# Kernel optimization log

Measured on AMD Instinct MI355X. Metric: run time of the kernel, lower is better.

The kernel has to match this reference:

```python
import jax, jax.numpy as jnp
import numpy as np

HID = 128
N_NODES = 50000
N_REL = 500
N_EDGES = 625000
BN_EPS = 1e-5
LRELU_SLOPE = 0.01


def _xavier(key, shape):
    fan_in, fan_out = shape[1], shape[0]
    std = float(np.sqrt(2.0 / (fan_in + fan_out)))
    return jax.random.normal(key, shape, dtype=jnp.float32) * std


def setup_inputs() -> dict:
    key = jax.random.key(0)
    ks = jax.random.split(key, 16)
    x = jax.random.normal(ks[0], (N_NODES, HID), dtype=jnp.float32)
    r = jax.random.normal(ks[1], (N_REL, HID), dtype=jnp.float32)
    que_context = jax.random.normal(ks[2], (1, HID), dtype=jnp.float32)
    fin_que = jax.random.normal(ks[3], (1, 1, HID), dtype=jnp.float32)
    edge_index = jax.random.randint(ks[4], (2, N_EDGES), 0, N_NODES, dtype=jnp.int64)
    edge_attr = jax.random.randint(ks[5], (N_EDGES,), 0, N_REL, dtype=jnp.int64)
    return {
        "x": x, "r": r, "que_context": que_context, "fin_que": fin_que,
        "edge_index": edge_index, "edge_attr": edge_attr,
        # mess_comp: Linear(2*hid, hid) + Tanh
        "W_mess": _xavier(ks[6], (HID, 2 * HID)), "b_mess": jnp.zeros((HID,), jnp.float32),
        # mess_atten_trans: Linear(2*hid, hid) + LeakyReLU
        "W_matt": _xavier(ks[7], (HID, 2 * HID)), "b_matt": jnp.zeros((HID,), jnp.float32),
        "mess_atten_weight": _xavier(ks[8], (1, HID)),
        # x_atten_trans: Linear(2*hid, hid) + LeakyReLU
        "W_xatt": _xavier(ks[9], (HID, 2 * HID)), "b_xatt": jnp.zeros((HID,), jnp.float32),
        "x_atten_weight": _xavier(ks[10], (1, HID)),
        # BatchNorm1d(hid) affine params (training-mode batch stats are used)
        "bn_gamma": jnp.ones((HID,), jnp.float32), "bn_beta": jnp.zeros((HID,), jnp.float32),
    }


def reference(x, r, que_context, fin_que, edge_index, edge_attr,
              W_mess, b_mess, W_matt, b_matt, mess_atten_weight,
              W_xatt, b_xatt, x_atten_weight, bn_gamma, bn_beta):
    n_nodes = x.shape[0]
    # BatchNorm1d over relation embeddings (training-mode: batch statistics, biased var)
    mu = jnp.mean(r, axis=0)
    var = jnp.mean(jnp.square(r - mu), axis=0)
    r = (r - mu) * jax.lax.rsqrt(var + BN_EPS) * bn_gamma + bn_beta

    head_ents, tail_ents = edge_index[0], edge_index[1]
    head_embeds = x[head_ents]            # [E, H]
    rel_embeds = r[edge_attr]             # [E, H]

    # message computation: Linear(2H->H) + tanh
    mess_in = jnp.concatenate([head_embeds, rel_embeds], axis=1)  # [E, 2H]
    mess = jnp.tanh(mess_in @ W_mess.T + b_mess)                  # [E, H]

    # message attention logits
    qc = jnp.broadcast_to(que_context, (mess.shape[0], que_context.shape[1]))
    mc = jnp.concatenate([mess, qc], axis=1) @ W_matt.T + b_matt
    mc = jax.nn.leaky_relu(mc, LRELU_SLOPE)
    mess_coeffs = jnp.sum(mess_atten_weight * mc, axis=1)         # [E]

    # segment softmax over tail_ents
    seg_max = jax.ops.segment_max(mess_coeffs, tail_ents, num_segments=n_nodes)
    mess_coeffs = jnp.exp(mess_coeffs - seg_max[tail_ents])
    seg_sum = jax.ops.segment_sum(mess_coeffs, tail_ents, num_segments=n_nodes)
    mess_weights = mess_coeffs / (seg_sum[tail_ents] + 1e-16)

    # weighted scatter-sum aggregation
    sum_mess = jax.ops.segment_sum(mess * mess_weights[:, None], tail_ents,
                                   num_segments=n_nodes)          # [N, H]

    # gating attention between x and aggregated messages
    pair = jnp.stack([x, sum_mess], axis=1)                       # [N, 2, H]
    fq = jnp.broadcast_to(fin_que, (n_nodes, 2, fin_que.shape[2]))
    xc = jnp.concatenate([pair, fq], axis=2)                      # [N, 2, 2H]
    xc = jax.nn.leaky_relu(jnp.einsum('nkc,hc->nkh', xc, W_xatt) + b_xatt, LRELU_SLOPE)
    x_coeffs = jnp.sum(x_atten_weight[None] * xc, axis=2)         # [N, 2]
    x_weight = jax.nn.softmax(x_coeffs, axis=1)
    x_out = x_weight[:, 0:1] * x + x_weight[:, 1:2] * sum_mess
    # dropout is identity (eval / p=0)
    return x_out, r
```

## Files before the change

kernel.cpp:

```cpp
#include <hip/hip_runtime.h>
#include <hip/hip_bf16.h>

#define HID 128
#define NN 50000
#define NR 500
#define NE 625000
#define LRELU 0.01f
#define SCAN_BLOCKS 196

typedef __hip_bfloat16 bf16;
typedef __attribute__((ext_vector_type(8))) short short8;
typedef __attribute__((ext_vector_type(4))) float float4_;

__device__ __forceinline__ float b2f(bf16 v) { return __bfloat162float(v); }
__device__ __forceinline__ bf16 f2b(float v) { return __float2bfloat16(v); }

__device__ __forceinline__ float san(float v) {
    return (v == v && v > -1e30f && v < 1e30f) ? v : 0.f;
}

__device__ __forceinline__ float ftanh(float a) {
    float e = __expf(2.f * a);
    return 1.f - 2.f * __builtin_amdgcn_rcpf(e + 1.f);
}

__device__ __forceinline__ float ldf(const void* p, int i, int f32) {
    return f32 ? ((const float*)p)[i] : b2f(((const bf16*)p)[i]);
}
__device__ __forceinline__ void stf(void* p, int i, float v, int f32) {
    if (f32) ((float*)p)[i] = v;
    else ((bf16*)p)[i] = f2b(v);
}

__device__ __forceinline__ int clampi(int v, int hi) {
    return v < 0 ? 0 : (v >= hi ? hi - 1 : v);
}
__device__ __forceinline__ int idx_at(const int* p, int i, int is64) {
    return p[is64 ? (2 * i) : i];
}

__device__ __forceinline__ unsigned short bfbits(float v) {
    bf16 h = f2b(v);
    return *(unsigned short*)&h;
}
__device__ __forceinline__ unsigned int packbf2(float a, float b) {
    return (unsigned int)bfbits(a) | ((unsigned int)bfbits(b) << 16);
}
__device__ __forceinline__ float bflo(unsigned int u) { return __uint_as_float(u << 16); }
__device__ __forceinline__ float bfhi(unsigned int u) { return __uint_as_float(u & 0xffff0000u); }

__device__ __forceinline__ float xorReduce16(float v) {
    v += __shfl_xor(v, 1, 64);
    v += __shfl_xor(v, 2, 64);
    v += __shfl_xor(v, 4, 64);
    v += __shfl_xor(v, 8, 64);
    return v;
}
__device__ __forceinline__ float waveMax(float v) {
#pragma unroll
    for (int o = 1; o < 64; o <<= 1) v = fmaxf(v, __shfl_xor(v, o, 64));
    return v;
}
__device__ __forceinline__ float waveSum(float v) {
#pragma unroll
    for (int o = 1; o < 64; o <<= 1) v += __shfl_xor(v, o, 64);
    return v;
}

__device__ __forceinline__ float dot8(const void* W, int row, int col, int f32,
                                      const float* vec) {
    float s;
    if (f32) {
        const float* p = (const float*)W + (size_t)row * 2 * HID + col;
        float4 a = *(const float4*)p;
        float4 b = *(const float4*)(p + 4);
        s = a.x * vec[0] + a.y * vec[1] + a.z * vec[2] + a.w * vec[3]
          + b.x * vec[4] + b.y * vec[5] + b.z * vec[6] + b.w * vec[7];
    } else {
        short8 v = *(const short8*)((const bf16*)W + (size_t)row * 2 * HID + col);
        s = 0.f;
#pragma unroll
        for (int i = 0; i < 8; ++i) {
            unsigned int u = ((unsigned int)(unsigned short)v[i]) << 16;
            s += __uint_as_float(u) * vec[i];
        }
    }
    return s;
}

struct DetectArr {
    const void* p[16];
    int sz[16];
    int kind[16];
};

__global__ void detect_all(DetectArr d, int* __restrict__ flags) {
    int b = blockIdx.x;
    int t = threadIdx.x;
    if (d.kind[b] == 1) {
        if (t < 64) {
            const int* q = (const int*)d.p[b];
            int o = q[2 * t + 1];
            unsigned long long bm = __ballot(o != 0);
            if (t == 0) flags[b] = (bm == 0ull) ? 1 : 0;
        }
        return;
    }
    __shared__ int sb[256], sf[256];
    const unsigned int* w = (const unsigned int*)d.p[b];
    int K = d.sz[b] >> 1;
    if (K > 4096) K = 4096;
    int bv = 0, fv = 0;
    for (int i = t; i < K; i += 256) {
        unsigned int x = w[i];
        unsigned int lo = x & 0xFFFFu, hi = x >> 16;
        if (lo == 0u) {
            if (hi) fv++;
        } else {
            unsigned int e = (lo >> 7) & 0xFFu;
            if (e >= 90u && e <= 160u) bv++;
            else fv++;
        }
    }
    sb[t] = bv; sf[t] = fv;
    __syncthreads();
    for (int o = 128; o > 0; o >>= 1) {
        if (t < o) { sb[t] += sb[t + o]; sf[t] += sf[t + o]; }
        __syncthreads();
    }
    if (t == 0) flags[b] = (sf[0] > sb[0]) ? 1 : 0;
}

__global__ void bn_stats(const void* __restrict__ r, const int* __restrict__ flags,
                         float* __restrict__ stats) {
    __shared__ float sb[256], sq[256];
    const int fr = flags[1];
    int h = blockIdx.x;
    int t = threadIdx.x;
    float s = 0.f, ss = 0.f;
    for (int i = t; i < NR; i += 256) {
        float v = ldf(r, i * HID + h, fr);
        s += v; ss += v * v;
    }
    sb[t] = s; sq[t] = ss;
    __syncthreads();
    for (int o = 128; o > 0; o >>= 1) {
        if (t < o) { sb[t] += sb[t + o]; sq[t] += sq[t + o]; }
        __syncthreads();
    }
    if (t == 0) {
        float mu = sb[0] / NR;
        float var = sq[0] / NR - mu * mu;
        if (var < 0.f) var = 0.f;
        stats[h] = mu;
        stats[HID + h] = rsqrtf(var + 1e-5f);
    }
}

__global__ void bn_apply(const void* __restrict__ r, const void* __restrict__ gamma,
                         const void* __restrict__ beta, const int* __restrict__ flags,
                         const float* __restrict__ stats,
                         float* __restrict__ rnorm, void* __restrict__ out_base) {
    const int fr = flags[1], fg = flags[14], fb = flags[15], fo = flags[0];
    int i = blockIdx.x * 256 + threadIdx.x;
    if (i >= NR * HID) return;
    int h = i & 127;
    float v = san((ldf(r, i, fr) - stats[h]) * stats[HID + h] * ldf(gamma, h, fg)
                  + ldf(beta, h, fb));
    rnorm[i] = v;
    stf(out_base, NN * HID + i, v, fo);
}

__global__ void precomp_kernel(const void* __restrict__ Wmatt, const void* __restrict__ bmatt,
                               const void* __restrict__ qc,
                               const void* __restrict__ Wxatt, const void* __restrict__ bxatt,
                               const void* __restrict__ fq, const int* __restrict__ flags,
                               float* __restrict__ cmatt, float* __restrict__ cxatt) {
    __shared__ float vs[HID];
    __shared__ float part[256];
    const void* W    = blockIdx.x ? Wxatt : Wmatt;
    const void* bias = blockIdx.x ? bxatt : bmatt;
    const void* vsrc = blockIdx.x ? fq : qc;
    float* out       = blockIdx.x ? cxatt : cmatt;
    const int fW = flags[blockIdx.x ? 11 : 8];
    const int fb = flags[blockIdx.x ? 12 : 9];
    const int fv = flags[blockIdx.x ? 3 : 2];
    int t = threadIdx.x;
    if (t < HID) vs[t] = ldf(vsrc, t, fv);
    __syncthreads();
    int h = t & 127, ks = t >> 7;
    float a = 0.f;
#pragma unroll
    for (int i = 0; i < 8; ++i)
        a += dot8(W, h, HID + ks * 64 + i * 8, fW, &vs[ks * 64 + i * 8]);
    part[t] = a;
    __syncthreads();
    if (t < HID) out[h] = san(part[h] + part[h + 128] + ldf(bias, h, fb));
}

__global__ void rm_kernel(const void* __restrict__ Wmess, const void* __restrict__ bmess,
                          const int* __restrict__ flags,
                          const float* __restrict__ rnorm, bf16* __restrict__ Rmb) {
    __shared__ float rl[2][HID];
    const int fW = flags[6], fb = flags[7];
    int t = threadIdx.x;
    int sub = t >> 7, h = t & 127;
    int rel = blockIdx.x * 2 + sub;
    rl[sub][h] = rnorm[rel * HID + h];
    __syncthreads();
    float a = ldf(bmess, h, fb);
#pragma unroll
    for (int i = 0; i < 16; ++i)
        a += dot8(Wmess, h, HID + i * 8, fW, &rl[sub][i * 8]);
    Rmb[rel * HID + h] = f2b(san(a));
}

#define MLDA 136

__device__ __forceinline__ short8 load_bfrag(const void* W, int n, int k0, int f32) {
    short8 b;
    if (f32) {
        const float* Wf = (const float*)W + (size_t)n * 2 * HID + k0;
        float4 u0 = *(const float4*)Wf;
        float4 u1 = *(const float4*)(Wf + 4);
        b[0] = (short)bfbits(u0.x); b[1] = (short)bfbits(u0.y);
        b[2] = (short)bfbits(u0.z); b[3] = (short)bfbits(u0.w);
        b[4] = (short)bfbits(u1.x); b[5] = (short)bfbits(u1.y);
        b[6] = (short)bfbits(u1.z); b[7] = (short)bfbits(u1.w);
    } else {
        b = *(const short8*)((const bf16*)W + (size_t)n * 2 * HID + k0);
    }
    return b;
}

__global__ __launch_bounds__(256, 4) void xm_mfma(const void* __restrict__ x,
                                                  const void* __restrict__ Wmess,
                                                  const int* __restrict__ flags,
                                                  bf16* __restrict__ Xmb) {
    __shared__ short ml[64 * MLDA];
    const int fx = flags[0], fW = flags[6];
    int tid = threadIdx.x;
    int l = tid & 63, w = tid >> 6;
    int quad = l >> 4, lo16 = l & 15;
    int nbase = w * 32;
    short8 bfr[2][4];
#pragma unroll
    for (int nt = 0; nt < 2; ++nt)
#pragma unroll
        for (int kk = 0; kk < 4; ++kk)
            bfr[nt][kk] = load_bfrag(Wmess, nbase + nt * 16 + lo16, kk * 32 + quad * 8, fW);

    const int ntiles = (NN + 63) / 64;
    for (int tile = blockIdx.x; tile < ntiles; tile += gridDim.x) {
        __syncthreads();
#pragma unroll
        for (int p = 0; p < 8; ++p) {
            int rl_ = p * 8 + (tid >> 5);
            int node = clampi(tile * 64 + rl_, NN);
            int k4 = (tid & 31) * 4;
            unsigned int o0, o1;
            if (fx) {
                float4 v = *(const float4*)((const float*)x + (size_t)node * HID + k4);
                o0 = packbf2(v.x, v.y);
                o1 = packbf2(v.z, v.w);
            } else {
                uint2 u = *(const uint2*)((const bf16*)x + (size_t)node * HID + k4);
                o0 = u.x; o1 = u.y;
            }
            unsigned int* dst = (unsigned int*)&ml[rl_ * MLDA + k4];
            dst[0] = o0; dst[1] = o1;
        }
        __syncthreads();
        float4_ acc[4][2];
#pragma unroll
        for (int mt = 0; mt < 4; ++mt)
#pragma unroll
            for (int nt = 0; nt < 2; ++nt)
                acc[mt][nt] = (float4_){0.f, 0.f, 0.f, 0.f};
#pragma unroll
        for (int kk = 0; kk < 4; ++kk) {
            short8 a[4];
#pragma unroll
            for (int mt = 0; mt < 4; ++mt)
                a[mt] = *(const short8*)&ml[(mt * 16 + lo16) * MLDA + kk * 32 + quad * 8];
#pragma unroll
            for (int mt = 0; mt < 4; ++mt)
#pragma unroll
                for (int nt = 0; nt < 2; ++nt)
                    acc[mt][nt] = __builtin_amdgcn_mfma_f32_16x16x32_bf16(
                        a[mt], bfr[nt][kk], acc[mt][nt], 0, 0, 0);
        }
#pragma unroll
        for (int mt = 0; mt < 4; ++mt)
#pragma unroll
            for (int nt = 0; nt < 2; ++nt)
#pragma unroll
                for (int r = 0; r < 4; ++r) {
                    int node = tile * 64 + mt * 16 + quad * 4 + r;
                    if (node < NN)
                        Xmb[node * HID + nbase + nt * 16 + lo16] = f2b(san(acc[mt][nt][r]));
                }
    }
}

__global__ __launch_bounds__(256, 6) void edge_coeff_mfma(
        const bf16* __restrict__ Xmb, const bf16* __restrict__ Rmb,
        const void* __restrict__ Wmatt, const float* __restrict__ cmatt,
        const void* __restrict__ maw, const unsigned int* __restrict__ hrcsr,
        const int* __restrict__ flags, float* __restrict__ ccsr) {
    __shared__ short ml[64 * MLDA];
    __shared__ float swave[4][64];
    const int fWm = flags[8], fmw = flags[10];
    int tid = threadIdx.x;
    int l = tid & 63, w = tid >> 6;
    int quad = l >> 4, lo16 = l & 15;
    int nbase = w * 32;
    short8 bfr[2][4];
#pragma unroll
    for (int nt = 0; nt < 2; ++nt)
#pragma unroll
        for (int kk = 0; kk < 4; ++kk)
            bfr[nt][kk] = load_bfrag(Wmatt, nbase + nt * 16 + lo16, kk * 32 + quad * 8, fWm);

    int n0 = nbase + lo16, n1 = n0 + 16;
    float c0 = cmatt[n0], c1 = cmatt[n1];
    float w0 = ldf(maw, n0, fmw), w1 = ldf(maw, n1, fmw);

    const int ntiles = (NE + 63) / 64;
    const int seg = tid & 15;
    const int rowsub = tid >> 4;
    for (int T = blockIdx.x; T < ntiles; T += gridDim.x) {
        __syncthreads();
#pragma unroll
        for (int p = 0; p < 4; ++p) {
            int el = p * 16 + rowsub;
            int slot = T * 64 + el;
            unsigned int hr = hrcsr[slot < NE ? slot : NE - 1];
            int head = hr & 0xffffu, rel = hr >> 16;
            int k8 = seg * 8;
            uint4 xv = *(const uint4*)&Xmb[head * HID + k8];
            uint4 rv = *(const uint4*)&Rmb[rel * HID + k8];
            uint4 o;
            o.x = packbf2(ftanh(bflo(xv.x) + bflo(rv.x)), ftanh(bfhi(xv.x) + bfhi(rv.x)));
            o.y = packbf2(ftanh(bflo(xv.y) + bflo(rv.y)), ftanh(bfhi(xv.y) + bfhi(rv.y)));
            o.z = packbf2(ftanh(bflo(xv.z) + bflo(rv.z)), ftanh(bfhi(xv.z) + bfhi(rv.z)));
            o.w = packbf2(ftanh(bflo(xv.w) + bflo(rv.w)), ftanh(bfhi(xv.w) + bfhi(rv.w)));
            *(uint4*)&ml[el * MLDA + k8] = o;
        }
        __syncthreads();
        float4_ acc[4][2];
#pragma unroll
        for (int mt = 0; mt < 4; ++mt)
#pragma unroll
            for (int nt = 0; nt < 2; ++nt)
                acc[mt][nt] = (float4_){0.f, 0.f, 0.f, 0.f};
#pragma unroll
        for (int kk = 0; kk < 4; ++kk) {
            short8 a[4];
#pragma unroll
            for (int mt = 0; mt < 4; ++mt)
                a[mt] = *(const short8*)&ml[(mt * 16 + lo16) * MLDA + kk * 32 + quad * 8];
#pragma unroll
            for (int mt = 0; mt < 4; ++mt)
#pragma unroll
                for (int nt = 0; nt < 2; ++nt)
                    acc[mt][nt] = __builtin_amdgcn_mfma_f32_16x16x32_bf16(
                        a[mt], bfr[nt][kk], acc[mt][nt], 0, 0, 0);
        }
#pragma unroll
        for (int mt = 0; mt < 4; ++mt)
#pragma unroll
            for (int r = 0; r < 4; ++r) {
                float z0 = acc[mt][0][r] + c0;
                z0 = z0 > 0.f ? z0 : LRELU * z0;
                float z1 = acc[mt][1][r] + c1;
                z1 = z1 > 0.f ? z1 : LRELU * z1;
                float s = w0 * z0 + w1 * z1;
                s = xorReduce16(s);
                if (lo16 == 0) swave[w][mt * 16 + quad * 4 + r] = s;
            }
        __syncthreads();
        if (tid < 64) {
            int slot = T * 64 + tid;
            if (slot < NE)
                ccsr[slot] = san(swave[0][tid] + swave[1][tid] + swave[2][tid] + swave[3][tid]);
        }
    }
}

__global__ __launch_bounds__(256, 4) void gate_mfma(
        const void* __restrict__ x, const bf16* __restrict__ smb,
        const void* __restrict__ Wxatt, const float* __restrict__ cxatt,
        const void* __restrict__ xaw, const int* __restrict__ flags,
        void* __restrict__ outx) {
    __shared__ short ml[64 * MLDA];
    __shared__ float swave[4][64];
    __shared__ float lgL[64];
    const int fx = flags[0], fWx = flags[11], fxw = flags[13], fo = flags[0];
    int tid = threadIdx.x;
    int l = tid & 63, w = tid >> 6;
    int quad = l >> 4, lo16 = l & 15;
    int nbase = w * 32;
    short8 bfr[2][4];
#pragma unroll
    for (int nt = 0; nt < 2; ++nt)
#pragma unroll
        for (int kk = 0; kk < 4; ++kk)
            bfr[nt][kk] = load_bfrag(Wxatt, nbase + nt * 16 + lo16, kk * 32 + quad * 8, fWx);

    int n0 = nbase + lo16, n1 = n0 + 16;
    float c0 = cxatt[n0], c1 = cxatt[n1];
    float w0 = ldf(xaw, n0, fxw), w1 = ldf(xaw, n1, fxw);

    const int ntiles = (NN + 31) / 32;
    for (int tile = blockIdx.x; tile < ntiles; tile += gridDim.x) {
        __syncthreads();
#pragma unroll
        for (int p = 0; p < 8; ++p) {
            int rl_ = p * 8 + (tid >> 5);
            int node = clampi(tile * 32 + (rl_ >> 1), NN);
            int k4 = (tid & 31) * 4;
            unsigned int o0, o1;
            if (rl_ & 1) {
                uint2 u = *(const uint2*)&smb[node * HID + k4];
                o0 = u.x; o1 = u.y;
            } else if (fx) {
                float4 v = *(const float4*)((const float*)x + (size_t)node * HID + k4);
                o0 = packbf2(v.x, v.y);
                o1 = packbf2(v.z, v.w);
            } else {
                uint2 u = *(const uint2*)((const bf16*)x + (size_t)node * HID + k4);
                o0 = u.x; o1 = u.y;
            }
            unsigned int* dst = (unsigned int*)&ml[rl_ * MLDA + k4];
            dst[0] = o0; dst[1] = o1;
        }
        __syncthreads();
        float4_ acc[4][2];
#pragma unroll
        for (int mt = 0; mt < 4; ++mt)
#pragma unroll
            for (int nt = 0; nt < 2; ++nt)
                acc[mt][nt] = (float4_){0.f, 0.f, 0.f, 0.f};
#pragma unroll
        for (int kk = 0; kk < 4; ++kk) {
            short8 a[4];
#pragma unroll
            for (int mt = 0; mt < 4; ++mt)
                a[mt] = *(const short8*)&ml[(mt * 16 + lo16) * MLDA + kk * 32 + quad * 8];
#pragma unroll
            for (int mt = 0; mt < 4; ++mt)
#pragma unroll
                for (int nt = 0; nt < 2; ++nt)
                    acc[mt][nt] = __builtin_amdgcn_mfma_f32_16x16x32_bf16(
                        a[mt], bfr[nt][kk], acc[mt][nt], 0, 0, 0);
        }
#pragma unroll
        for (int mt = 0; mt < 4; ++mt)
#pragma unroll
            for (int r = 0; r < 4; ++r) {
                float z0 = acc[mt][0][r] + c0;
                z0 = z0 > 0.f ? z0 : LRELU * z0;
                float z1 = acc[mt][1][r] + c1;
                z1 = z1 > 0.f ? z1 : LRELU * z1;
                float s = w0 * z0 + w1 * z1;
                s = xorReduce16(s);
                if (lo16 == 0) swave[w][mt * 16 + quad * 4 + r] = s;
            }
        __syncthreads();
        if (tid < 64)
            lgL[tid] = san(swave[0][tid] + swave[1][tid] + swave[2][tid] + swave[3][tid]);
        __syncthreads();
#pragma unroll
        for (int it = 0; it < 16; ++it) {
            int idx = tid + 256 * it;
            int nl = idx >> 7, h = idx & 127;
            int node = tile * 32 + nl;
            if (node < NN) {
                float g0 = lgL[2 * nl], g1 = lgL[2 * nl + 1];
                float mm = fmaxf(g0, g1);
                float e0 = __expf(g0 - mm), e1 = __expf(g1 - mm);
                float inv = __builtin_amdgcn_rcpf(e0 + e1);
                float xv = ldf(x, node * HID + h, fx);
                float sv = b2f(smb[node * HID + h]);
                stf(outx, node * HID + h, san((e0 * xv + e1 * sv) * inv), fo);
            }
        }
    }
}

__global__ void count_kernel(const int* __restrict__ ei, const int* __restrict__ flags,
                             int* __restrict__ counts) {
    const int is64e = flags[4];
    for (int e = blockIdx.x * blockDim.x + threadIdx.x; e < NE; e += gridDim.x * blockDim.x) {
        int tail = clampi(idx_at(ei, NE + e, is64e), NN);
        atomicAdd(&counts[tail], 1);
    }
}

__global__ void scan_phase1(const int* __restrict__ counts, int* __restrict__ offs,
                            int* __restrict__ bsum) {
    __shared__ int buf[256];
    int t = threadIdx.x;
    int i = blockIdx.x * 256 + t;
    int v = (i < NN) ? counts[i] : 0;
    buf[t] = v;
    __syncthreads();
    for (int off = 1; off < 256; off <<= 1) {
        int add = (t >= off) ? buf[t - off] : 0;
        __syncthreads();
        buf[t] += add;
        __syncthreads();
    }
    if (i < NN) offs[i] = buf[t] - v;
    if (t == 255) bsum[blockIdx.x] = buf[255];
}

__global__ void scan_phase2(int* __restrict__ bsum, int* __restrict__ bexc) {
    __shared__ int buf[256];
    int t = threadIdx.x;
    int v = (t < SCAN_BLOCKS) ? bsum[t] : 0;
    buf[t] = v;
    __syncthreads();
    for (int off = 1; off < 256; off <<= 1) {
        int add = (t >= off) ? buf[t - off] : 0;
        __syncthreads();
        buf[t] += add;
        __syncthreads();
    }
    if (t < SCAN_BLOCKS) bexc[t] = buf[t] - v;
    if (t == 255) bexc[SCAN_BLOCKS] = buf[255];
}

__global__ void scan_phase3(int* __restrict__ offs, int* __restrict__ cursor,
                            const int* __restrict__ bexc) {
    int i = blockIdx.x * 256 + threadIdx.x;
    if (i < NN) {
        int v = offs[i] + bexc[blockIdx.x];
        offs[i] = v;
        cursor[i] = v;
    }
    if (i == 0) offs[NN] = bexc[SCAN_BLOCKS];
}

__global__ void scatter_kernel(const int* __restrict__ ei, const int* __restrict__ ea,
                               const int* __restrict__ flags,
                               int* __restrict__ cursor, unsigned int* __restrict__ hrcsr) {
    const int is64e = flags[4], is64a = flags[5];
    for (int e = blockIdx.x * blockDim.x + threadIdx.x; e < NE; e += gridDim.x * blockDim.x) {
        int tail = clampi(idx_at(ei, NE + e, is64e), NN);
        int head = clampi(idx_at(ei, e, is64e), NN);
        int rel = clampi(idx_at(ea, e, is64a), NR);
        int p = atomicAdd(&cursor[tail], 1);
        if (p >= 0 && p < NE)
            hrcsr[p] = (unsigned int)head | ((unsigned int)rel << 16);
    }
}

__global__ __launch_bounds__(256, 8) void node_aggr_kernel(
        const bf16* __restrict__ Xmb, const bf16* __restrict__ Rmb,
        const int* __restrict__ offs, const unsigned int* __restrict__ hrcsr,
        const float* __restrict__ ccsr, bf16* __restrict__ smb) {
    int tid = threadIdx.x;
    int sub = tid >> 6;
    int lane = tid & 63;
    int node = blockIdx.x * 4 + sub;
    if (node >= NN) return;
    int s = offs[node], en = offs[node + 1];

    float m = -INFINITY;
    for (int i = s + lane; i < en; i += 64) m = fmaxf(m, ccsr[i]);
    m = waveMax(m);
    float lsum = 0.f;
    for (int i = s + lane; i < en; i += 64) lsum += __expf(ccsr[i] - m);
    lsum = waveSum(lsum);
    float inv = 1.f / (lsum + 1e-16f);

    const int col = lane * 2;
    float acc0 = 0.f, acc1 = 0.f;
    int i = s;
    for (; i + 2 <= en; i += 2) {
        unsigned int hr0 = hrcsr[i], hr1 = hrcsr[i + 1];
        float wg0 = __expf(ccsr[i] - m), wg1 = __expf(ccsr[i + 1] - m);
        unsigned int xv0 = *(const unsigned int*)&Xmb[(hr0 & 0xffffu) * HID + col];
        unsigned int rv0 = *(const unsigned int*)&Rmb[(hr0 >> 16) * HID + col];
        unsigned int xv1 = *(const unsigned int*)&Xmb[(hr1 & 0xffffu) * HID + col];
        unsigned int rv1 = *(const unsigned int*)&Rmb[(hr1 >> 16) * HID + col];
        acc0 += wg0 * ftanh(bflo(xv0) + bflo(rv0)) + wg1 * ftanh(bflo(xv1) + bflo(rv1));
        acc1 += wg0 * ftanh(bfhi(xv0) + bfhi(rv0)) + wg1 * ftanh(bfhi(xv1) + bfhi(rv1));
    }
    if (i < en) {
        unsigned int hr0 = hrcsr[i];
        float wg0 = __expf(ccsr[i] - m);
        unsigned int xv0 = *(const unsigned int*)&Xmb[(hr0 & 0xffffu) * HID + col];
        unsigned int rv0 = *(const unsigned int*)&Rmb[(hr0 >> 16) * HID + col];
        acc0 += wg0 * ftanh(bflo(xv0) + bflo(rv0));
        acc1 += wg0 * ftanh(bfhi(xv0) + bfhi(rv0));
    }
    *(unsigned int*)&smb[node * HID + col] = packbf2(san(acc0 * inv), san(acc1 * inv));
}

extern "C" void kernel_launch(void* const* d_in, const int* in_sizes, int n_in,
                              void* d_out, int out_size, void* d_ws, size_t ws_size,
                              hipStream_t stream) {
    const void* x     = d_in[0];
    const void* r     = d_in[1];
    const void* qc    = d_in[2];
    const void* fq    = d_in[3];
    const int*  ei    = (const int*)d_in[4];
    const int*  ea    = (const int*)d_in[5];
    const void* Wmess = d_in[6];
    const void* bmess = d_in[7];
    const void* Wmatt = d_in[8];
    const void* bmatt = d_in[9];
    const void* maw   = d_in[10];
    const void* Wxatt = d_in[11];
    const void* bxatt = d_in[12];
    const void* xaw   = d_in[13];
    const void* gamma = d_in[14];
    const void* beta  = d_in[15];

    int*          flags  = (int*)d_ws;
    int*          counts = flags + 16;
    int*          offs   = counts + NN;
    int*          cursor = offs + NN + 1;
    int*          bsum   = cursor + NN + 3;
    int*          bexc   = bsum + 256;
    unsigned int* hrcsr  = (unsigned int*)(bexc + 260);
    float*        ccsr   = (float*)(hrcsr + NE);
    float*        rnorm  = ccsr + NE;
    float*        stats  = rnorm + (size_t)NR * HID;
    float*        cmatt  = stats + 2 * HID;
    float*        cxatt  = cmatt + HID;
    bf16*         Rmb    = (bf16*)(cxatt + HID);
    bf16*         Xmb    = Rmb + (size_t)NR * HID;
    bf16*         smb    = Xmb + (size_t)NN * HID;

    hipMemsetAsync(counts, 0, NN * sizeof(int), stream);

    DetectArr da;
    const void* ps[16] = {x, r, qc, fq, ei, ea, Wmess, bmess, Wmatt, bmatt, maw,
                          Wxatt, bxatt, xaw, gamma, beta};
    int szs[16] = {NN * HID, NR * HID, HID, HID, 2 * NE, NE, 2 * HID * HID, HID,
                   2 * HID * HID, HID, HID, 2 * HID * HID, HID, HID, HID, HID};
    for (int i = 0; i < 16; ++i) {
        da.p[i] = ps[i];
        da.sz[i] = szs[i];
        da.kind[i] = (i == 4 || i == 5) ? 1 : 0;
    }
    detect_all<<<16, 256, 0, stream>>>(da, flags);

    bn_stats<<<HID, 256, 0, stream>>>(r, flags, stats);
    bn_apply<<<(NR * HID + 255) / 256, 256, 0, stream>>>(r, gamma, beta, flags, stats,
                                                         rnorm, d_out);
    precomp_kernel<<<2, 256, 0, stream>>>(Wmatt, bmatt, qc, Wxatt, bxatt, fq, flags,
                                          cmatt, cxatt);
    rm_kernel<<<NR / 2, 256, 0, stream>>>(Wmess, bmess, flags, rnorm, Rmb);
    xm_mfma<<<782, 256, 0, stream>>>(x, Wmess, flags, Xmb);
    count_kernel<<<1024, 256, 0, stream>>>(ei, flags, counts);
    scan_phase1<<<SCAN_BLOCKS, 256, 0, stream>>>(counts, offs, bsum);
    scan_phase2<<<1, 256, 0, stream>>>(bsum, bexc);
    scan_phase3<<<SCAN_BLOCKS, 256, 0, stream>>>(offs, cursor, bexc);
    scatter_kernel<<<1024, 256, 0, stream>>>(ei, ea, flags, cursor, hrcsr);
    edge_coeff_mfma<<<1536, 256, 0, stream>>>(Xmb, Rmb, Wmatt, cmatt, maw, hrcsr, flags,
                                              ccsr);
    node_aggr_kernel<<<(NN + 3) / 4, 256, 0, stream>>>(Xmb, Rmb, offs, hrcsr, ccsr, smb);
    gate_mfma<<<1563, 256, 0, stream>>>(x, smb, Wxatt, cxatt, xaw, flags, d_out);
}
```

Before: 409.9 us.

## Process edge coefficients in head-sorted order for gather locality, scatter to tail CSR

Builds a second CSR sorted by head node, with a slot map back to tail-CSR positions, and runs the edge coefficient kernel in head-sorted order. Consecutive edges then gather the same Xmb rows, which should improve cache reuse, and results are scattered into the tail-ordered ccsr array. The cost is an extra count/scan pass, more atomics in scatter, extra index arrays and scattered writes. Launch bounds occupancy and grid size are also raised.

```diff
diff --git a/kernel.cpp b/kernel.cpp
--- a/kernel.cpp
+++ b/kernel.cpp
@@ -303,10 +303,11 @@
     }
 }
 
-__global__ __launch_bounds__(256, 6) void edge_coeff_mfma(
+__global__ __launch_bounds__(256, 8) void edge_coeff_mfma(
         const bf16* __restrict__ Xmb, const bf16* __restrict__ Rmb,
         const void* __restrict__ Wmatt, const float* __restrict__ cmatt,
-        const void* __restrict__ maw, const unsigned int* __restrict__ hrcsr,
+        const void* __restrict__ maw, const unsigned int* __restrict__ hhr2,
+        const unsigned int* __restrict__ hslot,
         const int* __restrict__ flags, float* __restrict__ ccsr) {
     __shared__ short ml[64 * MLDA];
     __shared__ float swave[4][64];
@@ -334,8 +335,8 @@
 #pragma unroll
         for (int p = 0; p < 4; ++p) {
             int el = p * 16 + rowsub;
-            int slot = T * 64 + el;
-            unsigned int hr = hrcsr[slot < NE ? slot : NE - 1];
+            int i = T * 64 + el;
+            unsigned int hr = hhr2[i < NE ? i : NE - 1];
             int head = hr & 0xffffu, rel = hr >> 16;
             int k8 = seg * 8;
             uint4 xv = *(const uint4*)&Xmb[head * HID + k8];
@@ -381,9 +382,10 @@
             }
         __syncthreads();
         if (tid < 64) {
-            int slot = T * 64 + tid;
-            if (slot < NE)
-                ccsr[slot] = san(swave[0][tid] + swave[1][tid] + swave[2][tid] + swave[3][tid]);
+            int i = T * 64 + tid;
+            if (i < NE)
+                ccsr[hslot[i]] = san(swave[0][tid] + swave[1][tid]
+                                     + swave[2][tid] + swave[3][tid]);
         }
     }
 }
@@ -490,11 +492,13 @@
 }
 
 __global__ void count_kernel(const int* __restrict__ ei, const int* __restrict__ flags,
-                             int* __restrict__ counts) {
+                             int* __restrict__ countsT, int* __restrict__ countsH) {
     const int is64e = flags[4];
     for (int e = blockIdx.x * blockDim.x + threadIdx.x; e < NE; e += gridDim.x * blockDim.x) {
         int tail = clampi(idx_at(ei, NE + e, is64e), NN);
-        atomicAdd(&counts[tail], 1);
+        int head = clampi(idx_at(ei, e, is64e), NN);
+        atomicAdd(&countsT[tail], 1);
+        atomicAdd(&countsH[head], 1);
     }
 }
 
@@ -545,15 +549,23 @@
 
 __global__ void scatter_kernel(const int* __restrict__ ei, const int* __restrict__ ea,
                                const int* __restrict__ flags,
-                               int* __restrict__ cursor, unsigned int* __restrict__ hrcsr) {
+                               int* __restrict__ cursorT, int* __restrict__ cursorH,
+                               unsigned int* __restrict__ hrcsr,
+                               unsigned int* __restrict__ hhr2,
+                               unsigned int* __restrict__ hslot) {
     const int is64e = flags[4], is64a = flags[5];
     for (int e = blockIdx.x * blockDim.x + threadIdx.x; e < NE; e += gridDim.x * blockDim.x) {
         int tail = clampi(idx_at(ei, NE + e, is64e), NN);
         int head = clampi(idx_at(ei, e, is64e), NN);
         int rel = clampi(idx_at(ea, e, is64a), NR);
-        int p = atomicAdd(&cursor[tail], 1);
-        if (p >= 0 && p < NE)
-            hrcsr[p] = (unsigned int)head | ((unsigned int)rel << 16);
+        unsigned int hr = (unsigned int)head | ((unsigned int)rel << 16);
+        int p = atomicAdd(&cursorT[tail], 1);
+        if (p >= 0 && p < NE) hrcsr[p] = hr;
+        int q = atomicAdd(&cursorH[head], 1);
+        if (q >= 0 && q < NE) {
+            hhr2[q] = hr;
+            hslot[q] = (unsigned int)(p >= 0 && p < NE ? p : 0);
+        }
     }
 }
 
@@ -620,23 +632,30 @@
     const void* gamma = d_in[14];
     const void* beta  = d_in[15];
 
-    int*          flags  = (int*)d_ws;
-    int*          counts = flags + 16;
-    int*          offs   = counts + NN;
-    int*          cursor = offs + NN + 1;
-    int*          bsum   = cursor + NN + 3;
-    int*          bexc   = bsum + 256;
-    unsigned int* hrcsr  = (unsigned int*)(bexc + 260);
-    float*        ccsr   = (float*)(hrcsr + NE);
-    float*        rnorm  = ccsr + NE;
-    float*        stats  = rnorm + (size_t)NR * HID;
-    float*        cmatt  = stats + 2 * HID;
-    float*        cxatt  = cmatt + HID;
-    bf16*         Rmb    = (bf16*)(cxatt + HID);
-    bf16*         Xmb    = Rmb + (size_t)NR * HID;
-    bf16*         smb    = Xmb + (size_t)NN * HID;
-
-    hipMemsetAsync(counts, 0, NN * sizeof(int), stream);
+    int*          flags   = (int*)d_ws;
+    int*          counts  = flags + 16;
+    int*          hcounts = counts + NN;
+    int*          offs    = hcounts + NN;
+    int*          cursor  = offs + NN + 1;
+    int*          bsum    = cursor + NN + 3;
+    int*          bexc    = bsum + 256;
+    int*          hoffs   = bexc + 260;
+    int*          cursorH = hoffs + NN + 1;
+    int*          bsumH   = cursorH + NN + 3;
+    int*          bexcH   = bsumH + 256;
+    unsigned int* hrcsr   = (unsigned int*)(bexcH + 260);
+    unsigned int* hhr2    = hrcsr + NE;
+    unsigned int* hslot   = hhr2 + NE;
+    float*        ccsr    = (float*)(hslot + NE);
+    float*        rnorm   = ccsr + NE;
+    float*        stats   = rnorm + (size_t)NR * HID;
+    float*        cmatt   = stats + 2 * HID;
+    float*        cxatt   = cmatt + HID;
+    bf16*         Rmb     = (bf16*)(cxatt + HID);
+    bf16*         Xmb     = Rmb + (size_t)NR * HID;
+    bf16*         smb     = Xmb + (size_t)NN * HID;
+
+    hipMemsetAsync(counts, 0, 2 * NN * sizeof(int), stream);
 
     DetectArr da;
     const void* ps[16] = {x, r, qc, fq, ei, ea, Wmess, bmess, Wmatt, bmatt, maw,
@@ -657,13 +676,17 @@
                                           cmatt, cxatt);
     rm_kernel<<<NR / 2, 256, 0, stream>>>(Wmess, bmess, flags, rnorm, Rmb);
     xm_mfma<<<782, 256, 0, stream>>>(x, Wmess, flags, Xmb);
-    count_kernel<<<1024, 256, 0, stream>>>(ei, flags, counts);
+    count_kernel<<<1024, 256, 0, stream>>>(ei, flags, counts, hcounts);
     scan_phase1<<<SCAN_BLOCKS, 256, 0, stream>>>(counts, offs, bsum);
     scan_phase2<<<1, 256, 0, stream>>>(bsum, bexc);
     scan_phase3<<<SCAN_BLOCKS, 256, 0, stream>>>(offs, cursor, bexc);
-    scatter_kernel<<<1024, 256, 0, stream>>>(ei, ea, flags, cursor, hrcsr);
-    edge_coeff_mfma<<<1536, 256, 0, stream>>>(Xmb, Rmb, Wmatt, cmatt, maw, hrcsr, flags,
-                                              ccsr);
+    scan_phase1<<<SCAN_BLOCKS, 256, 0, stream>>>(hcounts, hoffs, bsumH);
+    scan_phase2<<<1, 256, 0, stream>>>(bsumH, bexcH);
+    scan_phase3<<<SCAN_BLOCKS, 256, 0, stream>>>(hoffs, cursorH, bexcH);
+    scatter_kernel<<<1024, 256, 0, stream>>>(ei, ea, flags, cursor, cursorH,
+                                             hrcsr, hhr2, hslot);
+    edge_coeff_mfma<<<2048, 256, 0, stream>>>(Xmb, Rmb, Wmatt, cmatt, maw, hhr2, hslot,
+                                              flags, ccsr);
     node_aggr_kernel<<<(NN + 3) / 4, 256, 0, stream>>>(Xmb, Rmb, offs, hrcsr, ccsr, smb);
     gate_mfma<<<1563, 256, 0, stream>>>(x, smb, Wxatt, cxatt, xaw, flags, d_out);
 }
```

Result: slower. 506.4 us (+23.6%).

## Group edges by head octant and materialize tanh messages for sequential aggregation

Applied to the files above, without the earlier changes.

Edges are bucketed into eight head-node octants via an extra count, scan and ballot-aggregated scatter, so each block of edge_coeff_mfma works on one octant and its Xmb gathers hit a smaller, more cache-resident slice. The edge kernel also writes the computed tanh messages in CSR order to a new 160MB messT buffer, and a new node_aggr_seq reads them contiguously instead of re-gathering Xmb/Rmb and recomputing tanh. This costs extra scatter traffic (ohr/oslot arrays), a scattered 160MB write and a 160MB read, and it depends on the workspace being large enough, falling back to the old path otherwise.

```diff
diff --git a/kernel.cpp b/kernel.cpp
--- a/kernel.cpp
+++ b/kernel.cpp
@@ -86,6 +86,10 @@
         }
     }
     return s;
+}
+
+__device__ __forceinline__ int octant_of(int head) {
+    return (head * 8) / NN;
 }
 
 struct DetectArr {
@@ -306,8 +310,10 @@
 __global__ __launch_bounds__(256, 6) void edge_coeff_mfma(
         const bf16* __restrict__ Xmb, const bf16* __restrict__ Rmb,
         const void* __restrict__ Wmatt, const float* __restrict__ cmatt,
-        const void* __restrict__ maw, const unsigned int* __restrict__ hrcsr,
-        const int* __restrict__ flags, float* __restrict__ ccsr) {
+        const void* __restrict__ maw, const unsigned int* __restrict__ ohr,
+        const int* __restrict__ oslot, const int* __restrict__ ooffs,
+        const int* __restrict__ flags, float* __restrict__ ccsr,
+        bf16* __restrict__ messT) {
     __shared__ short ml[64 * MLDA];
     __shared__ float swave[4][64];
     const int fWm = flags[8], fmw = flags[10];
@@ -326,16 +332,24 @@
     float c0 = cmatt[n0], c1 = cmatt[n1];
     float w0 = ldf(maw, n0, fmw), w1 = ldf(maw, n1, fmw);
 
-    const int ntiles = (NE + 63) / 64;
+    const int k = blockIdx.x & 7;
+    const int beg = ooffs[k], end = ooffs[k + 1];
+    const int tstride = gridDim.x >> 3;
     const int seg = tid & 15;
     const int rowsub = tid >> 4;
-    for (int T = blockIdx.x; T < ntiles; T += gridDim.x) {
-        __syncthreads();
+
+    for (int t = blockIdx.x >> 3;; t += tstride) {
+        int base = beg + t * 64;
+        if (base >= end) break;
+        __syncthreads();
+        int rslot[4];
 #pragma unroll
         for (int p = 0; p < 4; ++p) {
             int el = p * 16 + rowsub;
-            int slot = T * 64 + el;
-            unsigned int hr = hrcsr[slot < NE ? slot : NE - 1];
+            int i = base + el;
+            int idx = i < end ? i : end - 1;
+            unsigned int hr = ohr[idx];
+            rslot[p] = (i < end) ? oslot[i] : -1;
             int head = hr & 0xffffu, rel = hr >> 16;
             int k8 = seg * 8;
             uint4 xv = *(const uint4*)&Xmb[head * HID + k8];
@@ -367,6 +381,17 @@
                     acc[mt][nt] = __builtin_amdgcn_mfma_f32_16x16x32_bf16(
                         a[mt], bfr[nt][kk], acc[mt][nt], 0, 0, 0);
         }
+        if (messT) {
+#pragma unroll
+            for (int p = 0; p < 4; ++p) {
+                int slot = rslot[p];
+                if (slot >= 0) {
+                    int el = p * 16 + rowsub;
+                    *(uint4*)&messT[(size_t)slot * HID + seg * 8] =
+                        *(const uint4*)&ml[el * MLDA + seg * 8];
+                }
+            }
+        }
 #pragma unroll
         for (int mt = 0; mt < 4; ++mt)
 #pragma unroll
@@ -381,9 +406,12 @@
             }
         __syncthreads();
         if (tid < 64) {
-            int slot = T * 64 + tid;
-            if (slot < NE)
-                ccsr[slot] = san(swave[0][tid] + swave[1][tid] + swave[2][tid] + swave[3][tid]);
+            int i = base + tid;
+            if (i < end) {
+                int slot = oslot[i];
+                ccsr[slot] = san(swave[0][tid] + swave[1][tid]
+                                 + swave[2][tid] + swave[3][tid]);
+            }
         }
     }
 }
@@ -490,12 +518,19 @@
 }
 
 __global__ void count_kernel(const int* __restrict__ ei, const int* __restrict__ flags,
-                             int* __restrict__ counts) {
+                             int* __restrict__ counts, int* __restrict__ octcnt) {
+    __shared__ int oh[8];
     const int is64e = flags[4];
+    if (threadIdx.x < 8) oh[threadIdx.x] = 0;
+    __syncthreads();
     for (int e = blockIdx.x * blockDim.x + threadIdx.x; e < NE; e += gridDim.x * blockDim.x) {
         int tail = clampi(idx_at(ei, NE + e, is64e), NN);
+        int head = clampi(idx_at(ei, e, is64e), NN);
         atomicAdd(&counts[tail], 1);
-    }
+        atomicAdd(&oh[octant_of(head)], 1);
+    }
+    __syncthreads();
+    if (threadIdx.x < 8) atomicAdd(&octcnt[threadIdx.x], oh[threadIdx.x]);
 }
 
 __global__ void scan_phase1(const int* __restrict__ counts, int* __restrict__ offs,
@@ -543,18 +578,84 @@
     if (i == 0) offs[NN] = bexc[SCAN_BLOCKS];
 }
 
+__global__ void oct_scan(const int* __restrict__ octcnt, int* __restrict__ ooffs,
+                         int* __restrict__ octcur) {
+    if (threadIdx.x == 0) {
+        int acc = 0;
+        for (int i = 0; i < 8; ++i) { ooffs[i] = acc; octcur[i] = acc; acc += octcnt[i]; }
+        ooffs[8] = acc;
+    }
+}
+
 __global__ void scatter_kernel(const int* __restrict__ ei, const int* __restrict__ ea,
                                const int* __restrict__ flags,
-                               int* __restrict__ cursor, unsigned int* __restrict__ hrcsr) {
+                               int* __restrict__ cursorT, int* __restrict__ octcur,
+                               unsigned int* __restrict__ hrcsr,
+                               unsigned int* __restrict__ ohr, int* __restrict__ oslot) {
     const int is64e = flags[4], is64a = flags[5];
+    const int lane = threadIdx.x & 63;
     for (int e = blockIdx.x * blockDim.x + threadIdx.x; e < NE; e += gridDim.x * blockDim.x) {
         int tail = clampi(idx_at(ei, NE + e, is64e), NN);
         int head = clampi(idx_at(ei, e, is64e), NN);
         int rel = clampi(idx_at(ea, e, is64a), NR);
-        int p = atomicAdd(&cursor[tail], 1);
-        if (p >= 0 && p < NE)
-            hrcsr[p] = (unsigned int)head | ((unsigned int)rel << 16);
-    }
+        unsigned int hr = (unsigned int)head | ((unsigned int)rel << 16);
+        int p = atomicAdd(&cursorT[tail], 1);
+        if (p >= 0 && p < NE) hrcsr[p] = hr;
+        int o = octant_of(head);
+#pragma unroll
+        for (int oo = 0; oo < 8; ++oo) {
+            unsigned long long m = __ballot(o == oo);
+            if (o == oo) {
+                int leader = __ffsll((long long)m) - 1;
+                int pre = __popcll(m & ((1ull << lane) - 1ull));
+                int qb = 0;
+                if (lane == leader) qb = atomicAdd(&octcur[oo], __popcll(m));
+                qb = __shfl(qb, leader, 64);
+                int q = qb + pre;
+                if (q >= 0 && q < NE) {
+                    ohr[q] = hr;
+                    oslot[q] = (p >= 0 && p < NE) ? p : 0;
+                }
+            }
+        }
+    }
+}
+
+__global__ __launch_bounds__(256, 8) void node_aggr_seq(
+        const bf16* __restrict__ messT, const int* __restrict__ offs,
+        const float* __restrict__ ccsr, bf16* __restrict__ smb) {
+    int tid = threadIdx.x;
+    int sub = tid >> 6;
+    int lane = tid & 63;
+    int node = blockIdx.x * 4 + sub;
+    if (node >= NN) return;
+    int s = offs[node], en = offs[node + 1];
+
+    float m = -INFINITY;
+    for (int i = s + lane; i < en; i += 64) m = fmaxf(m, ccsr[i]);
+    m = waveMax(m);
+    float lsum = 0.f;
+    for (int i = s + lane; i < en; i += 64) lsum += __expf(ccsr[i] - m);
+    lsum = waveSum(lsum);
+    float inv = 1.f / (lsum + 1e-16f);
+
+    const int col = lane * 2;
+    float acc0 = 0.f, acc1 = 0.f;
+    int i = s;
+    for (; i + 2 <= en; i += 2) {
+        float wg0 = __expf(ccsr[i] - m), wg1 = __expf(ccsr[i + 1] - m);
+        unsigned int u0 = *(const unsigned int*)&messT[(size_t)i * HID + col];
+        unsigned int u1 = *(const unsigned int*)&messT[(size_t)(i + 1) * HID + col];
+        acc0 += wg0 * bflo(u0) + wg1 * bflo(u1);
+        acc1 += wg0 * bfhi(u0) + wg1 * bfhi(u1);
+    }
+    if (i < en) {
+        float wg0 = __expf(ccsr[i] - m);
+        unsigned int u0 = *(const unsigned int*)&messT[(size_t)i * HID + col];
+        acc0 += wg0 * bflo(u0);
+        acc1 += wg0 * bfhi(u0);
+    }
+    *(unsigned int*)&smb[node * HID + col] = packbf2(san(acc0 * inv), san(acc1 * inv));
 }
 
 __global__ __launch_bounds__(256, 8) void node_aggr_kernel(
@@ -578,18 +679,7 @@
 
     const int col = lane * 2;
     float acc0 = 0.f, acc1 = 0.f;
-    int i = s;
-    for (; i + 2 <= en; i += 2) {
-        unsigned int hr0 = hrcsr[i], hr1 = hrcsr[i + 1];
-        float wg0 = __expf(ccsr[i] - m), wg1 = __expf(ccsr[i + 1] - m);
-        unsigned int xv0 = *(const unsigned int*)&Xmb[(hr0 & 0xffffu) * HID + col];
-        unsigned int rv0 = *(const unsigned int*)&Rmb[(hr0 >> 16) * HID + col];
-        unsigned int xv1 = *(const unsigned int*)&Xmb[(hr1 & 0xffffu) * HID + col];
-        unsigned int rv1 = *(const unsigned int*)&Rmb[(hr1 >> 16) * HID + col];
-        acc0 += wg0 * ftanh(bflo(xv0) + bflo(rv0)) + wg1 * ftanh(bflo(xv1) + bflo(rv1));
-        acc1 += wg0 * ftanh(bfhi(xv0) + bfhi(rv0)) + wg1 * ftanh(bfhi(xv1) + bfhi(rv1));
-    }
-    if (i < en) {
+    for (int i = s; i < en; ++i) {
         unsigned int hr0 = hrcsr[i];
         float wg0 = __expf(ccsr[i] - m);
         unsigned int xv0 = *(const unsigned int*)&Xmb[(hr0 & 0xffffu) * HID + col];
@@ -620,23 +710,58 @@
     const void* gamma = d_in[14];
     const void* beta  = d_in[15];
 
-    int*          flags  = (int*)d_ws;
-    int*          counts = flags + 16;
-    int*          offs   = counts + NN;
-    int*          cursor = offs + NN + 1;
-    int*          bsum   = cursor + NN + 3;
-    int*          bexc   = bsum + 256;
-    unsigned int* hrcsr  = (unsigned int*)(bexc + 260);
-    float*        ccsr   = (float*)(hrcsr + NE);
-    float*        rnorm  = ccsr + NE;
-    float*        stats  = rnorm + (size_t)NR * HID;
-    float*        cmatt  = stats + 2 * HID;
-    float*        cxatt  = cmatt + HID;
-    bf16*         Rmb    = (bf16*)(cxatt + HID);
-    bf16*         Xmb    = Rmb + (size_t)NR * HID;
-    bf16*         smb    = Xmb + (size_t)NN * HID;
-
-    hipMemsetAsync(counts, 0, NN * sizeof(int), stream);
+    char* base = (char*)d_ws;
+    size_t off = 0;
+    auto alloc = [&](size_t bytes, size_t align) -> size_t {
+        off = (off + align - 1) & ~(align - 1);
+        size_t cur = off; off += bytes; return cur;
+    };
+    size_t o_flags  = alloc(16 * 4, 4);
+    size_t o_counts = alloc((size_t)NN * 4, 4);
+    size_t o_octcnt = alloc(8 * 4, 4);
+    size_t o_offs   = alloc((size_t)(NN + 1) * 4, 4);
+    size_t o_cursor = alloc((size_t)(NN + 3) * 4, 4);
+    size_t o_bsum   = alloc(256 * 4, 4);
+    size_t o_bexc   = alloc(264 * 4, 4);
+    size_t o_ooffs  = alloc(9 * 4, 4);
+    size_t o_octcur = alloc(8 * 4, 4);
+    size_t o_hrcsr  = alloc((size_t)NE * 4, 4);
+    size_t o_ohr    = alloc((size_t)NE * 4, 4);
+    size_t o_oslot  = alloc((size_t)NE * 4, 4);
+    size_t o_ccsr   = alloc((size_t)NE * 4, 4);
+    size_t o_rnorm  = alloc((size_t)NR * HID * 4, 4);
+    size_t o_stats  = alloc(2 * HID * 4, 4);
+    size_t o_cmatt  = alloc(HID * 4, 4);
+    size_t o_cxatt  = alloc(HID * 4, 4);
+    size_t o_Rmb    = alloc((size_t)NR * HID * 2, 4);
+    size_t o_Xmb    = alloc((size_t)NN * HID * 2, 4);
+    size_t o_smb    = alloc((size_t)NN * HID * 2, 4);
+    size_t o_messT  = alloc((size_t)NE * HID * 2, 256);
+    const bool useMess = ws_size >= off;
+
+    int*          flags  = (int*)(base + o_flags);
+    int*          counts = (int*)(base + o_counts);
+    int*          octcnt = (int*)(base + o_octcnt);
+    int*          offs   = (int*)(base + o_offs);
+    int*          cursor = (int*)(base + o_cursor);
+    int*          bsum   = (int*)(base + o_bsum);
+    int*          bexc   = (int*)(base + o_bexc);
+    int*          ooffs  = (int*)(base + o_ooffs);
+    int*          octcur = (int*)(base + o_octcur);
+    unsigned int* hrcsr  = (unsigned int*)(base + o_hrcsr);
+    unsigned int* ohr    = (unsigned int*)(base + o_ohr);
+    int*          oslot  = (int*)(base + o_oslot);
+    float*        ccsr   = (float*)(base + o_ccsr);
+    float*        rnorm  = (float*)(base + o_rnorm);
+    float*        stats  = (float*)(base + o_stats);
+    float*        cmatt  = (float*)(base + o_cmatt);
+    float*        cxatt  = (float*)(base + o_cxatt);
+    bf16*         Rmb    = (bf16*)(base + o_Rmb);
+    bf16*         Xmb    = (bf16*)(base + o_Xmb);
+    bf16*         smb    = (bf16*)(base + o_smb);
+    bf16*         messT  = useMess ? (bf16*)(base + o_messT) : (bf16*)nullptr;
+
+    hipMemsetAsync(counts, 0, ((size_t)NN + 8) * sizeof(int), stream);
 
     DetectArr da;
     const void* ps[16] = {x, r, qc, fq, ei, ea, Wmess, bmess, Wmatt, bmatt, maw,
@@ -657,13 +782,19 @@
                                           cmatt, cxatt);
     rm_kernel<<<NR / 2, 256, 0, stream>>>(Wmess, bmess, flags, rnorm, Rmb);
     xm_mfma<<<782, 256, 0, stream>>>(x, Wmess, flags, Xmb);
-    count_kernel<<<1024, 256, 0, stream>>>(ei, flags, counts);
+    count_kernel<<<1024, 256, 0, stream>>>(ei, flags, counts, octcnt);
     scan_phase1<<<SCAN_BLOCKS, 256, 0, stream>>>(counts, offs, bsum);
     scan_phase2<<<1, 256, 0, stream>>>(bsum, bexc);
     scan_phase3<<<SCAN_BLOCKS, 256, 0, stream>>>(offs, cursor, bexc);
-    scatter_kernel<<<1024, 256, 0, stream>>>(ei, ea, flags, cursor, hrcsr);
-    edge_coeff_mfma<<<1536, 256, 0, stream>>>(Xmb, Rmb, Wmatt, cmatt, maw, hrcsr, flags,
-                                              ccsr);
-    node_aggr_kernel<<<(NN + 3) / 4, 256, 0, stream>>>(Xmb, Rmb, offs, hrcsr, ccsr, smb);
+    oct_scan<<<1, 64, 0, stream>>>(octcnt, ooffs, octcur);
+    scatter_kernel<<<1024, 256, 0, stream>>>(ei, ea, flags, cursor, octcur,
+                                             hrcsr, ohr, oslot);
+    edge_coeff_mfma<<<1536, 256, 0, stream>>>(Xmb, Rmb, Wmatt, cmatt, maw, ohr, oslot,
+                                              ooffs, flags, ccsr, messT);
+    if (useMess)
+        node_aggr_seq<<<(NN + 3) / 4, 256, 0, stream>>>(messT, offs, ccsr, smb);
+    else
+        node_aggr_kernel<<<(NN + 3) / 4, 256, 0, stream>>>(Xmb, Rmb, offs, hrcsr, ccsr,
+                                                           smb);
     gate_mfma<<<1563, 256, 0, stream>>>(x, smb, Wxatt, cxatt, xaw, flags, d_out);
 }
```

Result: slower. 1.154 ms (+181.5%).

## Materialize per-edge messages in CSR order and aggregate them sequentially

Applied to the files above, without the earlier changes.

The edge coefficient kernel now also writes each computed tanh message row (bf16) into a CSR-ordered buffer. A new node aggregation kernel reads those contiguous rows instead of re-gathering X and R rows and recomputing tanh. This trades random gathers and recomputation for about 160 MB of extra sequential writes and reads. The new path is taken only when the workspace is large enough, otherwise the old kernel runs, now with an un-unrolled loop.

```diff
diff --git a/kernel.cpp b/kernel.cpp
--- a/kernel.cpp
+++ b/kernel.cpp
@@ -307,7 +307,8 @@
         const bf16* __restrict__ Xmb, const bf16* __restrict__ Rmb,
         const void* __restrict__ Wmatt, const float* __restrict__ cmatt,
         const void* __restrict__ maw, const unsigned int* __restrict__ hrcsr,
-        const int* __restrict__ flags, float* __restrict__ ccsr) {
+        const int* __restrict__ flags, float* __restrict__ ccsr,
+        bf16* __restrict__ messT) {
     __shared__ short ml[64 * MLDA];
     __shared__ float swave[4][64];
     const int fWm = flags[8], fmw = flags[10];
@@ -346,6 +347,8 @@
             o.z = packbf2(ftanh(bflo(xv.z) + bflo(rv.z)), ftanh(bfhi(xv.z) + bfhi(rv.z)));
             o.w = packbf2(ftanh(bflo(xv.w) + bflo(rv.w)), ftanh(bfhi(xv.w) + bfhi(rv.w)));
             *(uint4*)&ml[el * MLDA + k8] = o;
+            if (messT && slot < NE)
+                *(uint4*)&messT[(size_t)slot * HID + k8] = o;
         }
         __syncthreads();
         float4_ acc[4][2];
@@ -557,6 +560,43 @@
     }
 }
 
+__global__ __launch_bounds__(256, 8) void node_aggr_seq(
+        const bf16* __restrict__ messT, const int* __restrict__ offs,
+        const float* __restrict__ ccsr, bf16* __restrict__ smb) {
+    int tid = threadIdx.x;
+    int sub = tid >> 6;
+    int lane = tid & 63;
+    int node = blockIdx.x * 4 + sub;
+    if (node >= NN) return;
+    int s = offs[node], en = offs[node + 1];
+
+    float m = -INFINITY;
+    for (int i = s + lane; i < en; i += 64) m = fmaxf(m, ccsr[i]);
+    m = waveMax(m);
+    float lsum = 0.f;
+    for (int i = s + lane; i < en; i += 64) lsum += __expf(ccsr[i] - m);
+    lsum = waveSum(lsum);
+    float inv = 1.f / (lsum + 1e-16f);
+
+    const int col = lane * 2;
+    float acc0 = 0.f, acc1 = 0.f;
+    int i = s;
+    for (; i + 2 <= en; i += 2) {
+        float wg0 = __expf(ccsr[i] - m), wg1 = __expf(ccsr[i + 1] - m);
+        unsigned int u0 = *(const unsigned int*)&messT[(size_t)i * HID + col];
+        unsigned int u1 = *(const unsigned int*)&messT[(size_t)(i + 1) * HID + col];
+        acc0 += wg0 * bflo(u0) + wg1 * bflo(u1);
+        acc1 += wg0 * bfhi(u0) + wg1 * bfhi(u1);
+    }
+    if (i < en) {
+        float wg0 = __expf(ccsr[i] - m);
+        unsigned int u0 = *(const unsigned int*)&messT[(size_t)i * HID + col];
+        acc0 += wg0 * bflo(u0);
+        acc1 += wg0 * bfhi(u0);
+    }
+    *(unsigned int*)&smb[node * HID + col] = packbf2(san(acc0 * inv), san(acc1 * inv));
+}
+
 __global__ __launch_bounds__(256, 8) void node_aggr_kernel(
         const bf16* __restrict__ Xmb, const bf16* __restrict__ Rmb,
         const int* __restrict__ offs, const unsigned int* __restrict__ hrcsr,
@@ -578,18 +618,7 @@
 
     const int col = lane * 2;
     float acc0 = 0.f, acc1 = 0.f;
-    int i = s;
-    for (; i + 2 <= en; i += 2) {
-        unsigned int hr0 = hrcsr[i], hr1 = hrcsr[i + 1];
-        float wg0 = __expf(ccsr[i] - m), wg1 = __expf(ccsr[i + 1] - m);
-        unsigned int xv0 = *(const unsigned int*)&Xmb[(hr0 & 0xffffu) * HID + col];
-        unsigned int rv0 = *(const unsigned int*)&Rmb[(hr0 >> 16) * HID + col];
-        unsigned int xv1 = *(const unsigned int*)&Xmb[(hr1 & 0xffffu) * HID + col];
-        unsigned int rv1 = *(const unsigned int*)&Rmb[(hr1 >> 16) * HID + col];
-        acc0 += wg0 * ftanh(bflo(xv0) + bflo(rv0)) + wg1 * ftanh(bflo(xv1) + bflo(rv1));
-        acc1 += wg0 * ftanh(bfhi(xv0) + bfhi(rv0)) + wg1 * ftanh(bfhi(xv1) + bfhi(rv1));
-    }
-    if (i < en) {
+    for (int i = s; i < en; ++i) {
         unsigned int hr0 = hrcsr[i];
         float wg0 = __expf(ccsr[i] - m);
         unsigned int xv0 = *(const unsigned int*)&Xmb[(hr0 & 0xffffu) * HID + col];
@@ -620,23 +649,48 @@
     const void* gamma = d_in[14];
     const void* beta  = d_in[15];
 
-    int*          flags  = (int*)d_ws;
-    int*          counts = flags + 16;
-    int*          offs   = counts + NN;
-    int*          cursor = offs + NN + 1;
-    int*          bsum   = cursor + NN + 3;
-    int*          bexc   = bsum + 256;
-    unsigned int* hrcsr  = (unsigned int*)(bexc + 260);
-    float*        ccsr   = (float*)(hrcsr + NE);
-    float*        rnorm  = ccsr + NE;
-    float*        stats  = rnorm + (size_t)NR * HID;
-    float*        cmatt  = stats + 2 * HID;
-    float*        cxatt  = cmatt + HID;
-    bf16*         Rmb    = (bf16*)(cxatt + HID);
-    bf16*         Xmb    = Rmb + (size_t)NR * HID;
-    bf16*         smb    = Xmb + (size_t)NN * HID;
-
-    hipMemsetAsync(counts, 0, NN * sizeof(int), stream);
+    char* base = (char*)d_ws;
+    size_t off = 0;
+    auto alloc = [&](size_t bytes, size_t align) -> size_t {
+        off = (off + align - 1) & ~(align - 1);
+        size_t cur = off; off += bytes; return cur;
+    };
+    size_t o_flags  = alloc(16 * 4, 4);
+    size_t o_counts = alloc((size_t)NN * 4, 4);
+    size_t o_offs   = alloc((size_t)(NN + 1) * 4, 4);
+    size_t o_cursor = alloc((size_t)(NN + 3) * 4, 4);
+    size_t o_bsum   = alloc(256 * 4, 4);
+    size_t o_bexc   = alloc(264 * 4, 4);
+    size_t o_hrcsr  = alloc((size_t)NE * 4, 4);
+    size_t o_ccsr   = alloc((size_t)NE * 4, 4);
+    size_t o_rnorm  = alloc((size_t)NR * HID * 4, 4);
+    size_t o_stats  = alloc(2 * HID * 4, 4);
+    size_t o_cmatt  = alloc(HID * 4, 4);
+    size_t o_cxatt  = alloc(HID * 4, 4);
+    size_t o_Rmb    = alloc((size_t)NR * HID * 2, 4);
+    size_t o_Xmb    = alloc((size_t)NN * HID * 2, 4);
+    size_t o_smb    = alloc((size_t)NN * HID * 2, 4);
+    size_t o_messT  = alloc((size_t)NE * HID * 2, 256);
+    const bool useMess = ws_size >= off;
+
+    int*          flags  = (int*)(base + o_flags);
+    int*          counts = (int*)(base + o_counts);
+    int*          offs   = (int*)(base + o_offs);
+    int*          cursor = (int*)(base + o_cursor);
+    int*          bsum   = (int*)(base + o_bsum);
+    int*          bexc   = (int*)(base + o_bexc);
+    unsigned int* hrcsr  = (unsigned int*)(base + o_hrcsr);
+    float*        ccsr   = (float*)(base + o_ccsr);
+    float*        rnorm  = (float*)(base + o_rnorm);
+    float*        stats  = (float*)(base + o_stats);
+    float*        cmatt  = (float*)(base + o_cmatt);
+    float*        cxatt  = (float*)(base + o_cxatt);
+    bf16*         Rmb    = (bf16*)(base + o_Rmb);
+    bf16*         Xmb    = (bf16*)(base + o_Xmb);
+    bf16*         smb    = (bf16*)(base + o_smb);
+    bf16*         messT  = useMess ? (bf16*)(base + o_messT) : (bf16*)nullptr;
+
+    hipMemsetAsync(counts, 0, (size_t)NN * sizeof(int), stream);
 
     DetectArr da;
     const void* ps[16] = {x, r, qc, fq, ei, ea, Wmess, bmess, Wmatt, bmatt, maw,
@@ -663,7 +717,11 @@
     scan_phase3<<<SCAN_BLOCKS, 256, 0, stream>>>(offs, cursor, bexc);
     scatter_kernel<<<1024, 256, 0, stream>>>(ei, ea, flags, cursor, hrcsr);
     edge_coeff_mfma<<<1536, 256, 0, stream>>>(Xmb, Rmb, Wmatt, cmatt, maw, hrcsr, flags,
-                                              ccsr);
-    node_aggr_kernel<<<(NN + 3) / 4, 256, 0, stream>>>(Xmb, Rmb, offs, hrcsr, ccsr, smb);
+                                              ccsr, messT);
+    if (useMess)
+        node_aggr_seq<<<(NN + 3) / 4, 256, 0, stream>>>(messT, offs, ccsr, smb);
+    else
+        node_aggr_kernel<<<(NN + 3) / 4, 256, 0, stream>>>(Xmb, Rmb, offs, hrcsr, ccsr,
+                                                           smb);
     gate_mfma<<<1563, 256, 0, stream>>>(x, smb, Wxatt, cxatt, xaw, flags, d_out);
 }
```

New measurement: 422.4 us. +3.1%, slower.
